# Performance work log

Measured on AMD Instinct MI355X. Metric: run time of the kernel, lower is better.

Reference implementation:

```python
import jax, jax.numpy as jnp
import numpy as np

HEADS = 4


def setup_inputs() -> dict:
    key = jax.random.key(0)
    ks = jax.random.split(key, 6)
    b, c, d, h, w = 4, 512, 16, 16, 16
    x = jax.random.normal(ks[0], (b, c, d, h, w), dtype=jnp.float32)
    s = 0.02  # param init scale
    Wq = jax.random.normal(ks[1], (c, c), dtype=jnp.float32) * s
    Wk = jax.random.normal(ks[2], (c, c), dtype=jnp.float32) * s
    Wv = jax.random.normal(ks[3], (c, c), dtype=jnp.float32) * s
    Wproj = jax.random.normal(ks[4], (c, c), dtype=jnp.float32) * s
    bproj = jnp.zeros((c,), dtype=jnp.float32)
    return {"x": x, "Wq": Wq, "Wk": Wk, "Wv": Wv, "Wproj": Wproj, "bproj": bproj}


def reference(x, Wq, Wk, Wv, Wproj, bproj):
    b, c, d, h, w = x.shape
    N = d * h * w
    scale = (c // HEADS) ** -0.5  # module uses ch//heads for scale
    xf = x.reshape(b, c, N)  # (b, c, N)
    # 1x1 Conv1d == channel matmul
    q = jnp.einsum('oc,bcn->bon', Wq, xf)
    k = jnp.einsum('oc,bcn->bon', Wk, xf)
    v = jnp.einsum('oc,bcn->bon', Wv, xf)
    # Faithful to original (buggy) view: split SEQUENCE dim by heads -> (b, H, c, N//H)
    q = q.reshape(b, HEADS, c, N // HEADS)
    k = k.reshape(b, HEADS, c, N // HEADS)
    v = v.reshape(b, HEADS, c, N // HEADS)
    attn = jax.nn.softmax(jnp.einsum('bhqe,bhke->bhqk', q, k) * scale, axis=-1)
    out = jnp.einsum('bhqk,bhke->bhqe', attn, v)  # (b, H, c, N//H)
    out = jnp.swapaxes(out, 2, 3).reshape(b, c, N)  # matches transpose(2,3).view
    out = jnp.einsum('oc,bcn->bon', Wproj, out) + bproj[None, :, None]
    return out.reshape(b, c, d, h, w) + x
```

## Files before the change

### kernel.cpp

```cpp
#include <hip/hip_runtime.h>
#include <stdint.h>


typedef __attribute__((ext_vector_type(8))) short short8;
typedef __attribute__((ext_vector_type(4))) float f32x4;

typedef const __attribute__((address_space(1))) unsigned int* gas_ptr;
typedef __attribute__((address_space(3))) unsigned int* las_ptr;

#define ATTN_SCALE 0.08838834764831845f

__device__ __forceinline__ unsigned short f2bf(float f) {
    union { float f; unsigned int u; } c; c.f = f;
    unsigned int u = c.u;
    u += 0x7fffu + ((u >> 16) & 1u);
    return (unsigned short)(u >> 16);
}

__device__ __forceinline__ void gl_lds16(const void* g, void* l) {
    __builtin_amdgcn_global_load_lds((gas_ptr)(uintptr_t)g, (las_ptr)(uintptr_t)l,
                                     16, 0, 0);
}

template<int LDA, int LDB, int KDIM, bool PERMB = false>
__device__ __forceinline__ void mfma_core(
    const unsigned short* __restrict__ A,
    const unsigned short* __restrict__ B,
    int m0, int n0,
    unsigned short* __restrict__ sA, unsigned short* __restrict__ sB,
    f32x4 acc[4][4])
{
    const int tid  = threadIdx.x;
    const int lane = tid & 63, wave = tid >> 6;
    const int lr = lane >> 2, lc = lane & 3;
    const int lcs = lc ^ ((lr >> 1) & 3);
    const int wm = (wave & 1) * 64, wn = (wave >> 1) * 64;
    const int col = lane & 15, quad = lane >> 4;
    const int swz = (quad ^ ((col >> 1) & 3)) * 8;

    const unsigned short* ga = A + (size_t)(m0 + 32 * wave + lr) * LDA + lcs * 8;
    int rb0 = n0 + 32 * wave + lr;
    int rb1 = rb0 + 16;
    if (PERMB) {
        rb0 = 4 * (rb0 & 127) + (rb0 >> 7);
        rb1 = 4 * (rb1 & 127) + (rb1 >> 7);
    }
    const unsigned short* gb0 = B + (size_t)rb0 * LDB + lcs * 8;
    const unsigned short* gb1 = B + (size_t)rb1 * LDB + lcs * 8;

    const int wr0 = (32 * wave) * 32;
    const int wr1 = (32 * wave + 16) * 32;

    gl_lds16(ga,            sA + wr0);
    gl_lds16(ga + 16 * LDA, sA + wr1);
    gl_lds16(gb0,           sB + wr0);
    gl_lds16(gb1,           sB + wr1);

    constexpr int NK = KDIM / 32;
    for (int kk = 0; kk < NK; ++kk) {
        const int bo = (kk & 1) * 4096;
        if (kk + 1 < NK) {
            const int nb = ((kk + 1) & 1) * 4096;
            const int k0 = (kk + 1) * 32;
            gl_lds16(ga + k0,            sA + nb + wr0);
            gl_lds16(ga + k0 + 16 * LDA, sA + nb + wr1);
            gl_lds16(gb0 + k0,           sB + nb + wr0);
            gl_lds16(gb1 + k0,           sB + nb + wr1);
            asm volatile("s_waitcnt vmcnt(4)" ::: "memory");
        } else {
            asm volatile("s_waitcnt vmcnt(0)" ::: "memory");
        }
        __builtin_amdgcn_s_barrier();
        asm volatile("" ::: "memory");
        __builtin_amdgcn_sched_barrier(0);

        const unsigned short* bA = sA + bo;
        const unsigned short* bB = sB + bo;
        short8 af[4], bfv[4];
        #pragma unroll
        for (int i = 0; i < 4; ++i)
            af[i] = *(const short8*)&bA[(wm + i * 16 + col) * 32 + swz];
        #pragma unroll
        for (int j = 0; j < 4; ++j)
            bfv[j] = *(const short8*)&bB[(wn + j * 16 + col) * 32 + swz];
        #pragma unroll
        for (int i = 0; i < 4; ++i)
            #pragma unroll
            for (int j = 0; j < 4; ++j)
                acc[i][j] = __builtin_amdgcn_mfma_f32_16x16x32_bf16(
                    af[i], bfv[j], acc[i][j], 0, 0, 0);

        __builtin_amdgcn_s_barrier();
        asm volatile("" ::: "memory");
    }
}

__global__ __launch_bounds__(256)
void prep(const float* __restrict__ x,
          const float* __restrict__ Wq, const float* __restrict__ Wk,
          const float* __restrict__ Wv, const float* __restrict__ Wp,
          unsigned short* __restrict__ xT, unsigned short* __restrict__ Wb)
{
    if (blockIdx.z == 4) {
        const int idx = (blockIdx.y * 64 + blockIdx.x) * 256 + threadIdx.x;
        const int mat = idx >> 16;
        const int off = (idx & 65535) << 2;
        const float* src = (mat == 0 ? Wq : mat == 1 ? Wk : mat == 2 ? Wv : Wp) + off;
        const float4 f = *(const float4*)src;
        uint2 o;
        o.x = f2bf(f.x) | ((unsigned)f2bf(f.y) << 16);
        o.y = f2bf(f.z) | ((unsigned)f2bf(f.w) << 16);
        *(uint2*)&Wb[mat * 262144 + off] = o;
        return;
    }
    const int b = blockIdx.z;
    const int l = threadIdx.x & 63, w = threadIdx.x >> 6;
    const int n  = blockIdx.x * 64 + l;
    const int c0 = blockIdx.y * 32 + w * 8;
    const float* xp = x + (size_t)b * 2097152 + (size_t)c0 * 4096 + n;
    unsigned int p[4];
    #pragma unroll
    for (int j = 0; j < 4; ++j) {
        const unsigned short a  = f2bf(xp[(2 * j)     * 4096]);
        const unsigned short bb = f2bf(xp[(2 * j + 1) * 4096]);
        p[j] = a | ((unsigned)bb << 16);
    }
    uint4 v; v.x = p[0]; v.y = p[1]; v.z = p[2]; v.w = p[3];
    *(uint4*)&xT[(size_t)b * 2097152 + (size_t)n * 512 + c0] = v;
}

__global__ __launch_bounds__(256)
void gemm_qkv(const unsigned short* __restrict__ Wb,
              const unsigned short* __restrict__ xT,
              unsigned short* __restrict__ qb, unsigned short* __restrict__ kb,
              unsigned short* __restrict__ vT)
{
    __shared__ unsigned short sA[2 * 128 * 32], sB[2 * 128 * 32];

    const int z = blockIdx.z, wsel = z >> 2, b = z & 3;
    const unsigned short* A = Wb + wsel * 262144;
    const unsigned short* B = xT + (size_t)b * 2097152;
    const int m0 = blockIdx.y * 128, n0 = blockIdx.x * 128;

    f32x4 z4 = {0.f, 0.f, 0.f, 0.f};
    f32x4 acc[4][4];
    #pragma unroll
    for (int i = 0; i < 4; ++i)
        #pragma unroll
        for (int j = 0; j < 4; ++j) acc[i][j] = z4;

    mfma_core<512, 512, 512>(A, B, m0, n0, sA, sB, acc);

    const int lane = threadIdx.x & 63, wave = threadIdx.x >> 6;
    const int wm = (wave & 1) * 64, wn = (wave >> 1) * 64;
    const int col = lane & 15, quad = lane >> 4;

    if (wsel < 2) {
        unsigned short* C = (wsel == 0 ? qb : kb)
                          + (size_t)(b * 4 + (m0 >> 7)) * 524288;
        const int s  = n0 >> 10;
        const int e0 = (n0 & 1023) + wn;
        const int tq = wm + quad * 4;
        #pragma unroll
        for (int i = 0; i < 4; ++i) {
            #pragma unroll
            for (int j = 0; j < 4; ++j) {
                const int e  = e0 + j * 16 + col;
                const int Kc = e >> 5, qc = (e >> 3) & 3, el = e & 7;
                #pragma unroll
                for (int r = 0; r < 4; ++r) {
                    const int t = tq + i * 16 + r;
                    int R, cc;
                    if (wsel == 0) { R = t >> 2;           cc = 4 * (t & 3) + s; }
                    else           { R = s * 8 + (t >> 4); cc = t & 15; }
                    C[(R * 32 + Kc) * 512 + (qc * 16 + cc) * 8 + el] =
                        f2bf(acc[i][j][r]);
                }
            }
        }
    } else {
        const int h = m0 >> 7, s = n0 >> 10, e0 = n0 & 1023;
        unsigned short* dst = vT + (size_t)(b * 4 + h) * 524288 + s * 128;
        #pragma unroll
        for (int i = 0; i < 4; ++i) {
            const int kb2 = wm + i * 16 + quad * 4;
            #pragma unroll
            for (int j = 0; j < 4; ++j) {
                const int e = e0 + wn + j * 16 + col;
                uint2 o;
                o.x = f2bf(acc[i][j][0]) | ((unsigned)f2bf(acc[i][j][1]) << 16);
                o.y = f2bf(acc[i][j][2]) | ((unsigned)f2bf(acc[i][j][3]) << 16);
                *(uint2*)&dst[(size_t)e * 512 + kb2] = o;
            }
        }
    }
}

__global__ __launch_bounds__(512)
void gemm_qks(const unsigned short* __restrict__ qb,
              const unsigned short* __restrict__ kb,
              unsigned short* __restrict__ P)
{
    __shared__ float red[2][32][8];
    const int d = blockIdx.x;
    const int flat = (d & 7) * 32 + (d >> 3);
    const int rg = flat & 15, z = flat >> 4;
    const unsigned short* Aq = qb + (size_t)z * 524288;
    const unsigned short* Bk = kb + (size_t)z * 524288;
    unsigned short* Pz = P + (size_t)z * 262144;

    const int tid = threadIdx.x;
    const int lane = tid & 63, w = tid >> 6;
    const int col = lane & 15, quad = lane >> 4;

    const unsigned short* ap0 = Aq + (size_t)((rg * 2 + 0) * 32) * 512 + lane * 8;
    const unsigned short* ap1 = Aq + (size_t)((rg * 2 + 1) * 32) * 512 + lane * 8;
    const unsigned short* bp0 = Bk + (size_t)((w * 4 + 0) * 32) * 512 + lane * 8;
    const unsigned short* bp1 = bp0 + 16384;
    const unsigned short* bp2 = bp0 + 32768;
    const unsigned short* bp3 = bp0 + 49152;

    f32x4 z4 = {0.f, 0.f, 0.f, 0.f};
    f32x4 acc[2][4];
    #pragma unroll
    for (int f = 0; f < 2; ++f)
        #pragma unroll
        for (int g = 0; g < 4; ++g) acc[f][g] = z4;

    #pragma unroll 4
    for (int kk = 0; kk < 32; ++kk) {
        const int o = kk * 512;
        const short8 af0 = *(const short8*)(ap0 + o);
        const short8 af1 = *(const short8*)(ap1 + o);
        short8 bf[4];
        bf[0] = *(const short8*)(bp0 + o);
        bf[1] = *(const short8*)(bp1 + o);
        bf[2] = *(const short8*)(bp2 + o);
        bf[3] = *(const short8*)(bp3 + o);
        #pragma unroll
        for (int g = 0; g < 4; ++g)
            acc[0][g] = __builtin_amdgcn_mfma_f32_16x16x32_bf16(
                af0, bf[g], acc[0][g], 0, 0, 0);
        #pragma unroll
        for (int g = 0; g < 4; ++g)
            acc[1][g] = __builtin_amdgcn_mfma_f32_16x16x32_bf16(
                af1, bf[g], acc[1][g], 0, 0, 0);
    }

    float mx[2][4];
    #pragma unroll
    for (int f = 0; f < 2; ++f)
        #pragma unroll
        for (int r = 0; r < 4; ++r) {
            float m = acc[f][0][r];
            #pragma unroll
            for (int g = 1; g < 4; ++g) m = fmaxf(m, acc[f][g][r]);
            #pragma unroll
            for (int s = 1; s < 16; s <<= 1) m = fmaxf(m, __shfl_xor(m, s));
            mx[f][r] = m;
        }
    if (col == 0) {
        #pragma unroll
        for (int f = 0; f < 2; ++f)
            #pragma unroll
            for (int r = 0; r < 4; ++r)
                red[0][f * 16 + quad * 4 + r][w] = mx[f][r];
    }
    __syncthreads();
    float sm[2][4];
    #pragma unroll
    for (int f = 0; f < 2; ++f)
        #pragma unroll
        for (int r = 0; r < 4; ++r) {
            const int row = f * 16 + quad * 4 + r;
            float m = red[0][row][0];
            #pragma unroll
            for (int t = 1; t < 8; ++t) m = fmaxf(m, red[0][row][t]);
            float s = 0.f;
            #pragma unroll
            for (int g = 0; g < 4; ++g) {
                const float e = __expf((acc[f][g][r] - m) * ATTN_SCALE);
                acc[f][g][r] = e;
                s += e;
            }
            #pragma unroll
            for (int t = 1; t < 16; t <<= 1) s += __shfl_xor(s, t);
            sm[f][r] = s;
        }
    if (col == 0) {
        #pragma unroll
        for (int f = 0; f < 2; ++f)
            #pragma unroll
            for (int r = 0; r < 4; ++r)
                red[1][f * 16 + quad * 4 + r][w] = sm[f][r];
    }
    __syncthreads();
    #pragma unroll
    for (int f = 0; f < 2; ++f)
        #pragma unroll
        for (int r = 0; r < 4; ++r) {
            const int row = f * 16 + quad * 4 + r;
            float tot = red[1][row][0];
            #pragma unroll
            for (int t = 1; t < 8; ++t) tot += red[1][row][t];
            const float inv = 1.f / tot;
            unsigned short* op = Pz + (size_t)(rg * 32 + row) * 512
                               + w * 64 + col;
            #pragma unroll
            for (int g = 0; g < 4; ++g)
                op[g * 16] = f2bf(acc[f][g][r] * inv);
        }
}

__global__ __launch_bounds__(256)
void gemm_pv(const unsigned short* __restrict__ Pb,
             const unsigned short* __restrict__ vT,
             unsigned short* __restrict__ yT)
{
    __shared__ unsigned short sT[128 * 136];
    unsigned short* sA = sT;
    unsigned short* sB = sT + 8192;
    const int z = blockIdx.z, b = z >> 2, hh = z & 3;
    const unsigned short* A = Pb + (size_t)z * 262144;
    const unsigned short* B = vT + (size_t)z * 524288;
    unsigned short* yTb = yT + (size_t)b * 2097152;
    const int m0 = blockIdx.y * 128;
    const int n0 = blockIdx.x * 128;

    f32x4 z4 = {0.f, 0.f, 0.f, 0.f};
    f32x4 acc[4][4];
    #pragma unroll
    for (int i = 0; i < 4; ++i)
        #pragma unroll
        for (int j = 0; j < 4; ++j) acc[i][j] = z4;

    mfma_core<512, 512, 512>(A, B, m0, n0, sA, sB, acc);

    __syncthreads();

    const int tid = threadIdx.x;
    const int lane = tid & 63, wave = tid >> 6;
    const int wm = (wave & 1) * 64, wn = (wave >> 1) * 64;
    const int col = lane & 15, quad = lane >> 4;

    #pragma unroll
    for (int i = 0; i < 4; ++i)
        #pragma unroll
        for (int r = 0; r < 4; ++r) {
            const int rr = wm + i * 16 + quad * 4 + r;
            #pragma unroll
            for (int j = 0; j < 4; ++j)
                sT[rr * 136 + wn + j * 16 + col] = f2bf(acc[i][j][r]);
        }
    __syncthreads();

    #pragma unroll
    for (int k = 0; k < 4; ++k) {
        const int rid = k * 256 + tid;
        const int qq_l = rid >> 3, s = rid & 7;
        const unsigned short* Trow = sT + qq_l * 136;
        unsigned int p[8];
        #pragma unroll
        for (int t = 0; t < 8; ++t) {
            const unsigned int a  = Trow[s + 8 * (2 * t)];
            const unsigned int bb = Trow[s + 8 * (2 * t + 1)];
            p[t] = a | (bb << 16);
        }
        const size_t base = (size_t)((s << 9) + m0 + qq_l) * 512 + hh * 128 + (n0 >> 3);
        uint4 lo; lo.x = p[0]; lo.y = p[1]; lo.z = p[2]; lo.w = p[3];
        uint4 hi; hi.x = p[4]; hi.y = p[5]; hi.z = p[6]; hi.w = p[7];
        *(uint4*)&yTb[base]     = lo;
        *(uint4*)&yTb[base + 8] = hi;
    }
}

__global__ __launch_bounds__(256)
void gemm_proj(const unsigned short* __restrict__ Wpb,
               const unsigned short* __restrict__ yT,
               const float* __restrict__ bias, const float* __restrict__ x,
               float* __restrict__ out)
{
    __shared__ unsigned short sA[2 * 128 * 32], sB[2 * 128 * 32];
    const int b = blockIdx.z;
    const unsigned short* B = yT + (size_t)b * 2097152;
    const int m0 = blockIdx.y * 128, n0 = blockIdx.x * 128;

    f32x4 z4 = {0.f, 0.f, 0.f, 0.f};
    f32x4 acc[4][4];
    #pragma unroll
    for (int i = 0; i < 4; ++i)
        #pragma unroll
        for (int j = 0; j < 4; ++j) acc[i][j] = z4;

    mfma_core<512, 512, 512>(Wpb, B, m0, n0, sA, sB, acc);

    const int lane = threadIdx.x & 63, wave = threadIdx.x >> 6;
    const int wm = (wave & 1) * 64, wn = (wave >> 1) * 64;
    const int col = lane & 15, quad = lane >> 4;
    const size_t boff = (size_t)b * 2097152;
    #pragma unroll
    for (int i = 0; i < 4; ++i)
        #pragma unroll
        for (int r = 0; r < 4; ++r) {
            const int row = m0 + wm + i * 16 + quad * 4 + r;
            const float bi = bias[row];
            #pragma unroll
            for (int j = 0; j < 4; ++j) {
                const size_t idx = boff + (size_t)row * 4096 + n0 + wn + j * 16 + col;
                out[idx] = acc[i][j][r] + bi + x[idx];
            }
        }
}

extern "C" void kernel_launch(void* const* d_in, const int* in_sizes, int n_in,
                              void* d_out, int out_size, void* d_ws, size_t ws_size,
                              hipStream_t stream) {
    const float* x     = (const float*)d_in[0];
    const float* Wq    = (const float*)d_in[1];
    const float* Wk    = (const float*)d_in[2];
    const float* Wv    = (const float*)d_in[3];
    const float* Wproj = (const float*)d_in[4];
    const float* bproj = (const float*)d_in[5];
    float* out = (float*)d_out;

    char* w = (char*)d_ws;
    unsigned short* xT = (unsigned short*)(w + 0);
    unsigned short* qb = (unsigned short*)(w + 16777216);
    unsigned short* kb = (unsigned short*)(w + 33554432);
    unsigned short* vT = (unsigned short*)(w + 50331648);
    unsigned short* Pb = (unsigned short*)(w + 100663296);
    unsigned short* Wb = (unsigned short*)(w + 109051904);
    unsigned short* yT = xT;

    prep        <<<dim3(64, 16, 5),  256, 0, stream>>>(x, Wq, Wk, Wv, Wproj, xT, Wb);
    gemm_qkv    <<<dim3(32, 4, 12),  256, 0, stream>>>(Wb, xT, qb, kb, vT);
    gemm_qks    <<<dim3(256),        512, 0, stream>>>(qb, kb, Pb);
    gemm_pv     <<<dim3(8, 4, 16),   256, 0, stream>>>(Pb, vT, yT);
    gemm_proj   <<<dim3(32, 4, 4),   256, 0, stream>>>(Wb + 3 * 262144, yT, bproj, x, out);
}
```

Baseline: 191.0 us.

## Stage QKV GEMM epilogue through LDS for coalesced 16-byte stores, remap q layout

The QKV GEMM epilogue previously wrote scattered 2-byte (q/k) and 8-byte (v) stores directly from MFMA accumulators. It now stages the bf16 tile in shared memory, reusing the GEMM's staging buffer, and writes 16-byte vectorized rows so global stores coalesce. The q layout also changes (it no longer applies the per-row 4*(t&3)+s interleave), so the attention output write in a later kernel is adjusted to match the new row ordering. This adds extra barriers and LDS traffic, and it depends on the two layout changes staying consistent.

```diff
diff --git a/kernel.cpp b/kernel.cpp
--- a/kernel.cpp
+++ b/kernel.cpp
@@ -135,7 +135,9 @@
               unsigned short* __restrict__ qb, unsigned short* __restrict__ kb,
               unsigned short* __restrict__ vT)
 {
-    __shared__ unsigned short sA[2 * 128 * 32], sB[2 * 128 * 32];
+    __shared__ unsigned short sT[128 * 136];
+    unsigned short* sA = sT;
+    unsigned short* sB = sT + 8192;
 
     const int z = blockIdx.z, wsel = z >> 2, b = z & 3;
     const unsigned short* A = Wb + wsel * 262144;
@@ -151,47 +153,54 @@
 
     mfma_core<512, 512, 512>(A, B, m0, n0, sA, sB, acc);
 
-    const int lane = threadIdx.x & 63, wave = threadIdx.x >> 6;
+    __syncthreads();
+
+    const int tid = threadIdx.x;
+    const int lane = tid & 63, wave = tid >> 6;
     const int wm = (wave & 1) * 64, wn = (wave >> 1) * 64;
     const int col = lane & 15, quad = lane >> 4;
+    const int h = m0 >> 7, s = n0 >> 10;
 
     if (wsel < 2) {
+        #pragma unroll
+        for (int i = 0; i < 4; ++i)
+            #pragma unroll
+            for (int r = 0; r < 4; ++r) {
+                const int rr = wm + i * 16 + quad * 4 + r;
+                #pragma unroll
+                for (int j = 0; j < 4; ++j)
+                    sT[rr * 136 + wn + j * 16 + col] = f2bf(acc[i][j][r]);
+            }
+        __syncthreads();
         unsigned short* C = (wsel == 0 ? qb : kb)
-                          + (size_t)(b * 4 + (m0 >> 7)) * 524288;
-        const int s  = n0 >> 10;
-        const int e0 = (n0 & 1023) + wn;
-        const int tq = wm + quad * 4;
-        #pragma unroll
-        for (int i = 0; i < 4; ++i) {
-            #pragma unroll
-            for (int j = 0; j < 4; ++j) {
-                const int e  = e0 + j * 16 + col;
-                const int Kc = e >> 5, qc = (e >> 3) & 3, el = e & 7;
+                          + (size_t)(b * 4 + h) * 524288;
+        const int bKc = (n0 & 1023) >> 5;
+        const int u = tid & 15, v = (tid >> 4) & 3, wv = tid >> 6;
+        unsigned short* dst = C + (size_t)(s * 256 + bKc + wv) * 512
+                            + (v * 16 + u) * 8;
+        const unsigned short* src = sT + u * 136 + wv * 32 + v * 8;
+        #pragma unroll
+        for (int k = 0; k < 8; ++k)
+            *(uint4*)(dst + k * 16384) = *(const uint4*)(src + k * 2176);
+    } else {
+        #pragma unroll
+        for (int i = 0; i < 4; ++i)
+            #pragma unroll
+            for (int r = 0; r < 4; ++r) {
+                const int rr = wm + i * 16 + quad * 4 + r;
                 #pragma unroll
-                for (int r = 0; r < 4; ++r) {
-                    const int t = tq + i * 16 + r;
-                    int R, cc;
-                    if (wsel == 0) { R = t >> 2;           cc = 4 * (t & 3) + s; }
-                    else           { R = s * 8 + (t >> 4); cc = t & 15; }
-                    C[(R * 32 + Kc) * 512 + (qc * 16 + cc) * 8 + el] =
-                        f2bf(acc[i][j][r]);
-                }
+                for (int j = 0; j < 4; ++j)
+                    sT[(wn + j * 16 + col) * 136 + rr] = f2bf(acc[i][j][r]);
             }
-        }
-    } else {
-        const int h = m0 >> 7, s = n0 >> 10, e0 = n0 & 1023;
+        __syncthreads();
+        const int e0 = n0 & 1023;
         unsigned short* dst = vT + (size_t)(b * 4 + h) * 524288 + s * 128;
-        #pragma unroll
-        for (int i = 0; i < 4; ++i) {
-            const int kb2 = wm + i * 16 + quad * 4;
-            #pragma unroll
-            for (int j = 0; j < 4; ++j) {
-                const int e = e0 + wn + j * 16 + col;
-                uint2 o;
-                o.x = f2bf(acc[i][j][0]) | ((unsigned)f2bf(acc[i][j][1]) << 16);
-                o.y = f2bf(acc[i][j][2]) | ((unsigned)f2bf(acc[i][j][3]) << 16);
-                *(uint2*)&dst[(size_t)e * 512 + kb2] = o;
-            }
+        const int u = tid & 15, rsel = tid >> 4;
+        #pragma unroll
+        for (int k = 0; k < 8; ++k) {
+            const int ee = rsel + k * 16;
+            *(uint4*)&dst[(size_t)(e0 + ee) * 512 + u * 8] =
+                *(const uint4*)&sT[ee * 136 + u * 8];
         }
     }
 }
@@ -354,6 +363,7 @@
         }
     __syncthreads();
 
+    const int sblk = m0 >> 7;
     #pragma unroll
     for (int k = 0; k < 4; ++k) {
         const int rid = k * 256 + tid;
@@ -366,7 +376,8 @@
             const unsigned int bb = Trow[s + 8 * (2 * t + 1)];
             p[t] = a | (bb << 16);
         }
-        const size_t base = (size_t)((s << 9) + m0 + qq_l) * 512 + hh * 128 + (n0 >> 3);
+        const size_t base = (size_t)((s << 9) + 4 * qq_l + sblk) * 512
+                          + hh * 128 + (n0 >> 3);
         uint4 lo; lo.x = p[0]; lo.y = p[1]; lo.z = p[2]; lo.w = p[3];
         uint4 hi; hi.x = p[4]; hi.y = p[5]; hi.z = p[6]; hi.w = p[7];
         *(uint4*)&yTb[base]     = lo;
```

Result: faster. 185.7 us, median of 3 (-2.8%).
